# Optimization experiments

Measured on AMD Instinct MI355X. Metric: run time of the kernel, lower is better.

The kernel has to match this reference:

```python
import jax, jax.numpy as jnp
import numpy as np

B, N, F_IN = 8, 1024, 128
H, F_OUT = 4, 64
NEG_INF = -9e15


def setup_inputs() -> dict:
    key = jax.random.key(0)
    k1, k2, k3, k4 = jax.random.split(key, 4)
    x = jax.random.normal(k1, (B, N, F_IN), dtype=jnp.float32)
    adj = jax.random.randint(k2, (B, N, N), 0, 2, dtype=jnp.int32)
    W = jax.random.normal(k3, (F_IN, H * F_OUT), dtype=jnp.float32) * 0.05
    a = jax.random.normal(k4, (H, 2 * F_OUT), dtype=jnp.float32)
    return {"x": x, "adj": adj, "W": W, "a": a}


def reference(x, adj, W, a):
    # x: [B,N,F_in], adj: [B,N,N], W: [F_in, H*F_out], a: [H, 2*F_out]
    Bs, Ns, _ = x.shape
    Hh = a.shape[0]
    Fo = a.shape[1] // 2
    h = (x @ W).reshape(Bs, Ns, Hh, Fo)            # [B,N,H,F]
    # e_{bnmh} = a . cat(h_i, h_j) = a_src . h_n + a_dst . h_m  (no O(N^2) concat)
    a_src, a_dst = a[:, :Fo], a[:, Fo:]
    e_src = jnp.einsum('bnhf,hf->bnh', h, a_src)    # [B,N,H]
    e_dst = jnp.einsum('bmhf,hf->bmh', h, a_dst)    # [B,N,H]
    e = e_src[:, :, None, :] + e_dst[:, None, :, :]  # [B,N,N,H]
    e = jax.nn.leaky_relu(e, negative_slope=0.2)
    e = jnp.where(adj[..., None] > 0, e, NEG_INF)
    attention = jax.nn.softmax(e, axis=2)           # softmax over neighbors m
    h_prime = jnp.einsum('bnmh,bmhf->bnhf', attention, h)
    return h_prime.mean(axis=2)                     # [B,N,F_out]
```

## Files before the change

### kernel.cpp

```cpp
#include <hip/hip_runtime.h>
#include <hip/hip_bf16.h>
#include <math.h>

#define Bsz 8
#define Nsz 1024
#define FIN 128
#define Hh  4
#define FO  64
#define COLS 256
#define TN  16
#define TM  32
#define BN  (Bsz*Nsz)
#define SHIFT 12.0f
#define HSTR 40
#define PSTR 136

typedef __attribute__((ext_vector_type(8))) short short8;
typedef __attribute__((ext_vector_type(4))) float f32x4;
typedef __attribute__((ext_vector_type(2))) float f32x2;

static __device__ inline ushort f2bf(float f) {
    uint u = __float_as_uint(f);
    u += 0x7FFFu + ((u >> 16) & 1u);
    return (ushort)(u >> 16);
}
static __device__ inline uint cvt_pk2(float lo, float hi) {
    union { __hip_bfloat162 h; uint u; } cv;
    cv.h = __float22bfloat162_rn(float2{lo, hi});
    return cv.u;
}

__global__ __launch_bounds__(256) void gat_prep(const float* __restrict__ W,
                                                ushort* __restrict__ Wt)
{
    const int g = blockIdx.x * 256 + threadIdx.x;
    const int n = g >> 3, kc = (g & 7) * 16;
    ushort u[16];
    #pragma unroll
    for (int i = 0; i < 16; i++) u[i] = f2bf(W[(kc + i) * COLS + n]);
    int4* dst = (int4*)(Wt + n * FIN + kc);
    dst[0] = ((int4*)u)[0];
    dst[1] = ((int4*)u)[1];
}

__global__ __launch_bounds__(256) void gat_proj(
    const float* __restrict__ x, const ushort* __restrict__ Wt,
    const float* __restrict__ a, ushort* __restrict__ h_gB,
    float* __restrict__ es_g, float* __restrict__ ed_g)
{
    const int j    = threadIdx.x;
    const int w    = j >> 6, lane = j & 63, quad = lane >> 4, n16 = lane & 15;
    const int b    = blockIdx.x >> 6, mt16 = blockIdx.x & 63;
    const long rowbase = (long)b * Nsz + mt16 * 16;

    short8 bfr[4][4];
    #pragma unroll
    for (int kk = 0; kk < 4; kk++)
        #pragma unroll
        for (int c4 = 0; c4 < 4; c4++)
            bfr[kk][c4] = *(const short8*)(Wt + (w*64 + c4*16 + n16) * FIN + kk*32 + quad*8);

    short8 af[4];
    const float* xr = x + (rowbase + n16) * FIN + quad * 8;
    #pragma unroll
    for (int kk = 0; kk < 4; kk++) {
        float4 v0 = *(const float4*)(xr + kk*32);
        float4 v1 = *(const float4*)(xr + kk*32 + 4);
        union { uint u[4]; short8 s; } pk;
        pk.u[0] = cvt_pk2(v0.x, v0.y); pk.u[1] = cvt_pk2(v0.z, v0.w);
        pk.u[2] = cvt_pk2(v1.x, v1.y); pk.u[3] = cvt_pk2(v1.z, v1.w);
        af[kk] = pk.s;
    }

    f32x4 acc[4];
    #pragma unroll
    for (int c4 = 0; c4 < 4; c4++)
        #pragma unroll
        for (int r = 0; r < 4; r++) acc[c4][r] = 0.f;

    #pragma unroll
    for (int kk = 0; kk < 4; kk++)
        #pragma unroll
        for (int c4 = 0; c4 < 4; c4++)
            acc[c4] = __builtin_amdgcn_mfma_f32_16x16x32_bf16(af[kk], bfr[kk][c4], acc[c4], 0, 0, 0);

    const int mtile = mt16 >> 1;
    const int kbase = (mt16 & 1) * 16 + quad * 4;
    #pragma unroll
    for (int c4 = 0; c4 < 4; c4++) {
        uint2 pk;
        pk.x = cvt_pk2(acc[c4][0], acc[c4][1]);
        pk.y = cvt_pk2(acc[c4][2], acc[c4][3]);
        const int c = w*64 + c4*16 + n16;
        *(uint2*)(h_gB + (((long)(b*32 + mtile) * COLS + c) * 32 + kbase)) = pk;
    }

    float aS[4], aD[4];
    #pragma unroll
    for (int c4 = 0; c4 < 4; c4++) {
        aS[c4] = a[w * (2*FO) + c4*16 + n16];
        aD[c4] = a[w * (2*FO) + FO + c4*16 + n16];
    }
    #pragma unroll
    for (int reg = 0; reg < 4; reg++) {
        float ps = 0.f, pd = 0.f;
        #pragma unroll
        for (int c4 = 0; c4 < 4; c4++) {
            ps = fmaf(acc[c4][reg], aS[c4], ps);
            pd = fmaf(acc[c4][reg], aD[c4], pd);
        }
        #pragma unroll
        for (int off = 1; off < 16; off <<= 1) {
            ps += __shfl_xor(ps, off, 64);
            pd += __shfl_xor(pd, off, 64);
        }
        if (n16 == 0) {
            const long row = rowbase + quad*4 + reg;
            es_g[(long)w * BN + row] = ps;
            ed_g[(long)w * BN + row] = pd;
        }
    }
}

__global__ __launch_bounds__(256, 2) void gat_attn(
    const int* __restrict__ adj, const ushort* __restrict__ h_gB,
    const float* __restrict__ es_g, const float* __restrict__ ed_g,
    float* __restrict__ out)
{
    __shared__ ushort hT[2][COLS * HSTR];
    __shared__ ushort pT[2][TN * PSTR];
    __shared__ float  l_lds[TN * Hh];

    const int j    = threadIdx.x;
    const int w    = j >> 6, lane = j & 63, quad = lane >> 4, n16 = lane & 15;
    const int mi   = lane & 31, hh = lane >> 5;
    const int b    = blockIdx.y;
    const int n0   = blockIdx.x * TN;
    const long rowb = (long)b * Nsz + n0;

    f32x2 es2[4];
    #pragma unroll
    for (int r4 = 0; r4 < 4; r4++)
        es2[r4] = (f32x2){ es_g[(long)(hh*2 + 0) * BN + rowb + w*4 + r4],
                           es_g[(long)(hh*2 + 1) * BN + rowb + w*4 + r4] };

    f32x4 acc[4];
    #pragma unroll
    for (int c4 = 0; c4 < 4; c4++)
        #pragma unroll
        for (int r = 0; r < 4; r++) acc[c4][r] = 0.f;

    f32x2 l2p[4];
    #pragma unroll
    for (int r4 = 0; r4 < 4; r4++) l2p[r4] = (f32x2){0.f, 0.f};

    short8 hr[2][4]; int ar[2][4]; f32x2 edr[2];
    const short8* hb8 = (const short8*)h_gB;

#define PREFETCH(t, S) {                                                        \
    const short8* g = hb8 + (long)(b*32 + (t)) * 1024;                          \
    hr[S][0] = g[j];     hr[S][1] = g[j+256];                                   \
    hr[S][2] = g[j+512]; hr[S][3] = g[j+768];                                   \
    const int m0p = (t) * TM;                                                   \
    _Pragma("unroll")                                                           \
    for (int r4 = 0; r4 < 4; r4++)                                              \
        ar[S][r4] = adj[(rowb + w*4 + r4) * (long)Nsz + m0p + mi];              \
    edr[S] = (f32x2){ ed_g[(long)(hh*2 + 0) * BN + (long)b * Nsz + m0p + mi],   \
                      ed_g[(long)(hh*2 + 1) * BN + (long)b * Nsz + m0p + mi] }; }

#define STAGE(buf, S) {                                                         \
    _Pragma("unroll")                                                           \
    for (int i = 0; i < 4; i++) {                                               \
        const int s = j + 256*i;                                                \
        *(short8*)(&hT[buf][(s >> 2) * HSTR + (s & 3) * 8]) = hr[S][i]; } }

#define PHASE_S(buf, S) {                                                       \
    _Pragma("unroll")                                                           \
    for (int r4 = 0; r4 < 4; r4++) {                                            \
        f32x2 s2 = es2[r4] + edr[S];                                            \
        s2 = __builtin_elementwise_max(s2, s2 * 0.2f);                          \
        s2 = s2 - SHIFT;                                                        \
        float e0 = __expf(s2.x), e1 = __expf(s2.y);                             \
        const bool keep = ar[S][r4] > 0;                                        \
        uint pk = cvt_pk2(keep ? e0 : 0.f, keep ? e1 : 0.f);                    \
        pT[buf][(w*4 + r4) * PSTR + (hh*2 + 0) * TM + mi] = (ushort)(pk & 0xFFFFu); \
        pT[buf][(w*4 + r4) * PSTR + (hh*2 + 1) * TM + mi] = (ushort)(pk >> 16); \
        l2p[r4] += (f32x2){ __uint_as_float(pk << 16),                          \
                            __uint_as_float(pk & 0xFFFF0000u) }; } }

#define PHASE_A(buf) {                                                          \
    short8 afp = *(const short8*)(&pT[buf][n16 * PSTR + w * TM + quad * 8]);    \
    _Pragma("unroll")                                                           \
    for (int c4 = 0; c4 < 4; c4++) {                                            \
        short8 bfv = *(const short8*)(&hT[buf][(w*64 + c4*16 + n16) * HSTR + quad * 8]); \
        acc[c4] = __builtin_amdgcn_mfma_f32_16x16x32_bf16(afp, bfv, acc[c4], 0, 0, 0); } }

    PREFETCH(0, 0); PREFETCH(1, 1);
    STAGE(0, 0); PHASE_S(0, 0);
    PREFETCH(2, 0);
    __syncthreads();

    for (int tt = 0; tt < 16; tt++) {
        const int t0 = 2 * tt;
        if (t0 < 31) {
            STAGE(1, 1); PHASE_S(1, 1);
            if (t0 + 3 < 32) PREFETCH(t0 + 3, 1);
        }
        PHASE_A(0);
        __syncthreads();
        if (t0 + 1 < 31) {
            STAGE(0, 0); PHASE_S(0, 0);
            if (t0 + 4 < 32) PREFETCH(t0 + 4, 0);
        }
        PHASE_A(1);
        __syncthreads();
    }

    #pragma unroll
    for (int r4 = 0; r4 < 4; r4++)
        #pragma unroll
        for (int ii = 0; ii < 2; ii++) {
            float lp = ii ? l2p[r4].y : l2p[r4].x;
            #pragma unroll
            for (int off = 1; off < 32; off <<= 1) lp += __shfl_xor(lp, off, 64);
            if (mi == 0) l_lds[(w*4 + r4) * Hh + hh*2 + ii] = lp;
        }
    __syncthreads();

    float* o_lds = (float*)&hT[0][0];
    float rinv[4];
    #pragma unroll
    for (int reg = 0; reg < 4; reg++)
        rinv[reg] = 0.25f / l_lds[(quad*4 + reg) * Hh + w];
    #pragma unroll
    for (int c4 = 0; c4 < 4; c4++)
        #pragma unroll
        for (int reg = 0; reg < 4; reg++)
            o_lds[(w * TN + quad*4 + reg) * FO + c4*16 + n16] = acc[c4][reg] * rinv[reg];
    __syncthreads();

    {
        const int f2 = j & 63, rb = j >> 6;
        #pragma unroll
        for (int i = 0; i < 4; i++) {
            const int r = i*4 + rb;
            const float sum = o_lds[(0*TN + r)*FO + f2] + o_lds[(1*TN + r)*FO + f2]
                            + o_lds[(2*TN + r)*FO + f2] + o_lds[(3*TN + r)*FO + f2];
            out[(rowb + r) * FO + f2] = sum;
        }
    }
#undef PREFETCH
#undef STAGE
#undef PHASE_S
#undef PHASE_A
}

extern "C" void kernel_launch(void* const* d_in, const int* in_sizes, int n_in,
                              void* d_out, int out_size, void* d_ws, size_t ws_size,
                              hipStream_t stream) {
    const float* x   = (const float*)d_in[0];
    const int*   adj = (const int*)d_in[1];
    const float* W   = (const float*)d_in[2];
    const float* a   = (const float*)d_in[3];
    float* out = (float*)d_out;

    ushort* Wt   = (ushort*)d_ws;
    ushort* h_gB = Wt + (size_t)COLS * FIN;
    float*  es_g = (float*)(h_gB + (size_t)BN * COLS);
    float*  ed_g = es_g + (size_t)Hh * BN;

    gat_prep<<<dim3(8),            dim3(256), 0, stream>>>(W, Wt);
    gat_proj<<<dim3(Bsz*Nsz/16),   dim3(256), 0, stream>>>(x, Wt, a, h_gB, es_g, ed_g);
    gat_attn<<<dim3(Nsz/TN, Bsz),  dim3(256), 0, stream>>>(adj, h_gB, es_g, ed_g, out);
}
```

Measured before the change: 116.1 us.

## Split attention over neighbor dimension into four partial blocks plus combine kernel

Splits the neighbor (m) loop of the attention kernel across four blocks via a z grid dimension. Each block writes unnormalized partial accumulators and row sums to workspace, and a new combine kernel sums the partials, normalizes per head and averages. The fixed shift exponent makes the partials directly additive. The aim is more blocks to fill the GPU (512 blocks was low occupancy for 256 CUs). The cost is extra global traffic for the partials (about 8MB written and re-read), one more launch, and a larger workspace requirement.

Result: slower. 120.8 us (+4.0%).

```diff
diff --git a/kernel.cpp b/kernel.cpp
--- a/kernel.cpp
+++ b/kernel.cpp
@@ -14,6 +14,8 @@
 #define SHIFT 12.0f
 #define HSTR 40
 #define PSTR 136
+#define MSPLIT 4
+#define TPS  8
 
 typedef __attribute__((ext_vector_type(8))) short short8;
 typedef __attribute__((ext_vector_type(4))) float f32x4;
@@ -125,16 +127,16 @@
 __global__ __launch_bounds__(256, 2) void gat_attn(
     const int* __restrict__ adj, const ushort* __restrict__ h_gB,
     const float* __restrict__ es_g, const float* __restrict__ ed_g,
-    float* __restrict__ out)
+    float* __restrict__ oP, float* __restrict__ lP)
 {
     __shared__ ushort hT[2][COLS * HSTR];
     __shared__ ushort pT[2][TN * PSTR];
-    __shared__ float  l_lds[TN * Hh];
 
     const int j    = threadIdx.x;
     const int w    = j >> 6, lane = j & 63, quad = lane >> 4, n16 = lane & 15;
     const int mi   = lane & 31, hh = lane >> 5;
     const int b    = blockIdx.y;
+    const int half = blockIdx.z;
     const int n0   = blockIdx.x * TN;
     const long rowb = (long)b * Nsz + n0;
 
@@ -158,10 +160,11 @@
     const short8* hb8 = (const short8*)h_gB;
 
 #define PREFETCH(t, S) {                                                        \
-    const short8* g = hb8 + (long)(b*32 + (t)) * 1024;                          \
+    const int gt_ = half * TPS + (t);                                           \
+    const short8* g = hb8 + (long)(b*32 + gt_) * 1024;                          \
     hr[S][0] = g[j];     hr[S][1] = g[j+256];                                   \
     hr[S][2] = g[j+512]; hr[S][3] = g[j+768];                                   \
-    const int m0p = (t) * TM;                                                   \
+    const int m0p = gt_ * TM;                                                   \
     _Pragma("unroll")                                                           \
     for (int r4 = 0; r4 < 4; r4++)                                              \
         ar[S][r4] = adj[(rowb + w*4 + r4) * (long)Nsz + m0p + mi];              \
@@ -200,22 +203,23 @@
     PREFETCH(2, 0);
     __syncthreads();
 
-    for (int tt = 0; tt < 16; tt++) {
+    for (int tt = 0; tt < TPS/2; tt++) {
         const int t0 = 2 * tt;
-        if (t0 < 31) {
+        if (t0 < TPS - 1) {
             STAGE(1, 1); PHASE_S(1, 1);
-            if (t0 + 3 < 32) PREFETCH(t0 + 3, 1);
+            if (t0 + 3 < TPS) PREFETCH(t0 + 3, 1);
         }
         PHASE_A(0);
         __syncthreads();
-        if (t0 + 1 < 31) {
+        if (t0 + 1 < TPS - 1) {
             STAGE(0, 0); PHASE_S(0, 0);
-            if (t0 + 4 < 32) PREFETCH(t0 + 4, 0);
+            if (t0 + 4 < TPS) PREFETCH(t0 + 4, 0);
         }
         PHASE_A(1);
         __syncthreads();
     }
 
+    const long pbase = (long)((half * Bsz + b) * 64 + blockIdx.x);
     #pragma unroll
     for (int r4 = 0; r4 < 4; r4++)
         #pragma unroll
@@ -223,36 +227,44 @@
             float lp = ii ? l2p[r4].y : l2p[r4].x;
             #pragma unroll
             for (int off = 1; off < 32; off <<= 1) lp += __shfl_xor(lp, off, 64);
-            if (mi == 0) l_lds[(w*4 + r4) * Hh + hh*2 + ii] = lp;
-        }
-    __syncthreads();
-
-    float* o_lds = (float*)&hT[0][0];
-    float rinv[4];
-    #pragma unroll
-    for (int reg = 0; reg < 4; reg++)
-        rinv[reg] = 0.25f / l_lds[(quad*4 + reg) * Hh + w];
+            if (mi == 0)
+                lP[pbase * (Hh*TN) + (hh*2 + ii) * TN + w*4 + r4] = lp;
+        }
     #pragma unroll
     for (int c4 = 0; c4 < 4; c4++)
         #pragma unroll
         for (int reg = 0; reg < 4; reg++)
-            o_lds[(w * TN + quad*4 + reg) * FO + c4*16 + n16] = acc[c4][reg] * rinv[reg];
-    __syncthreads();
-
-    {
-        const int f2 = j & 63, rb = j >> 6;
-        #pragma unroll
-        for (int i = 0; i < 4; i++) {
-            const int r = i*4 + rb;
-            const float sum = o_lds[(0*TN + r)*FO + f2] + o_lds[(1*TN + r)*FO + f2]
-                            + o_lds[(2*TN + r)*FO + f2] + o_lds[(3*TN + r)*FO + f2];
-            out[(rowb + r) * FO + f2] = sum;
-        }
-    }
+            oP[pbase * (Hh*TN*FO) + ((w*TN + quad*4 + reg) * FO) + c4*16 + n16] = acc[c4][reg];
 #undef PREFETCH
 #undef STAGE
 #undef PHASE_S
 #undef PHASE_A
+}
+
+__global__ __launch_bounds__(256) void gat_comb(
+    const float* __restrict__ oP, const float* __restrict__ lP,
+    float* __restrict__ out)
+{
+    const int nt = blockIdx.x, b = blockIdx.y;
+    const int j = threadIdx.x;
+    #pragma unroll
+    for (int k = 0; k < 4; k++) {
+        const int idx = j + k * 256;
+        const int r = idx >> 6, f = idx & 63;
+        float sum = 0.f;
+        #pragma unroll
+        for (int hd = 0; hd < Hh; hd++) {
+            float v = 0.f, l = 0.f;
+            #pragma unroll
+            for (int half = 0; half < MSPLIT; half++) {
+                const long base = (long)((half * Bsz + b) * 64 + nt);
+                v += oP[base * (Hh*TN*FO) + (hd*TN + r) * FO + f];
+                l += lP[base * (Hh*TN)   + hd*TN + r];
+            }
+            sum += v / l;
+        }
+        out[((long)b * Nsz + nt*16 + r) * FO + f] = sum * 0.25f;
+    }
 }
 
 extern "C" void kernel_launch(void* const* d_in, const int* in_sizes, int n_in,
@@ -268,8 +280,11 @@
     ushort* h_gB = Wt + (size_t)COLS * FIN;
     float*  es_g = (float*)(h_gB + (size_t)BN * COLS);
     float*  ed_g = es_g + (size_t)Hh * BN;
-
-    gat_prep<<<dim3(8),            dim3(256), 0, stream>>>(W, Wt);
-    gat_proj<<<dim3(Bsz*Nsz/16),   dim3(256), 0, stream>>>(x, Wt, a, h_gB, es_g, ed_g);
-    gat_attn<<<dim3(Nsz/TN, Bsz),  dim3(256), 0, stream>>>(adj, h_gB, es_g, ed_g, out);
-}
+    float*  oP   = ed_g + (size_t)Hh * BN;
+    float*  lP   = oP + (size_t)MSPLIT * Bsz * 64 * (Hh*TN*FO);
+
+    gat_prep<<<dim3(8),                    dim3(256), 0, stream>>>(W, Wt);
+    gat_proj<<<dim3(Bsz*Nsz/16),           dim3(256), 0, stream>>>(x, Wt, a, h_gB, es_g, ed_g);
+    gat_attn<<<dim3(Nsz/TN, Bsz, MSPLIT),  dim3(256), 0, stream>>>(adj, h_gB, es_g, ed_g, oP, lP);
+    gat_comb<<<dim3(Nsz/TN, Bsz),          dim3(256), 0, stream>>>(oP, lP, out);
+}
```
